# Kernel tuning notes

Hardware: AMD Instinct MI355X
Metric: run time of the kernel (lower is better)

## Reference

```python
import jax, jax.numpy as jnp
import numpy as np

N = 20000      # nodes
E = 320000     # directed edges (self-loops added inside reference)
DIN = 128      # input_dim
HID = 64       # hidden_dim
H = 4          # num_heads
B = 16         # graphs in batch
OUT = 1        # output_dim
NEG_SLOPE = 0.2


def setup_inputs() -> dict:
    key = jax.random.key(0)
    ks = jax.random.split(key, 20)
    p = lambda k, shape: (jax.random.normal(k, shape, jnp.float32) * 0.05)
    x = jax.random.normal(ks[0], (N, DIN), jnp.float32)
    edge_index = jax.random.randint(ks[1], (2, E), 0, N, dtype=jnp.int64)
    batch = jnp.sort(jax.random.randint(ks[2], (N,), 0, B, dtype=jnp.int64))
    return {
        "x": x, "edge_index": edge_index, "batch": batch,
        # gat1: DIN -> (H, HID), concat
        "W1": p(ks[3], (DIN, H * HID)), "as1": p(ks[4], (H, HID)), "ad1": p(ks[5], (H, HID)), "b1": jnp.zeros((H * HID,), jnp.float32),
        # gat2: H*HID -> (H, HID), concat
        "W2": p(ks[6], (H * HID, H * HID)), "as2": p(ks[7], (H, HID)), "ad2": p(ks[8], (H, HID)), "b2": jnp.zeros((H * HID,), jnp.float32),
        # gat_out: H*HID -> (1, HID), mean (concat=False)
        "W3": p(ks[9], (H * HID, HID)), "as3": p(ks[10], (1, HID)), "ad3": p(ks[11], (1, HID)), "b3": jnp.zeros((HID,), jnp.float32),
        "wp": p(ks[12], (HID, 1)), "bp": jnp.zeros((1,), jnp.float32),
        "wr": p(ks[13], (HID, OUT)), "br": jnp.zeros((OUT,), jnp.float32),
    }


def _gat_layer(x, W, a_src, a_dst, bias, src, dst, heads, concat):
    n = x.shape[0]
    h = (x @ W).reshape(n, heads, -1)                      # [N,H,C]
    e_src = (h * a_src).sum(-1)                            # [N,H]
    e_dst = (h * a_dst).sum(-1)                            # [N,H]
    e = jax.nn.leaky_relu(e_src[src] + e_dst[dst], NEG_SLOPE)  # [Etot,H]
    # segment softmax over destination node (self-loops guarantee non-empty)
    m = jax.ops.segment_max(e, dst, num_segments=n)
    e = jnp.exp(e - m[dst])
    den = jax.ops.segment_sum(e, dst, num_segments=n)
    alpha = e / den[dst]                                   # [Etot,H]
    out = jax.ops.segment_sum(h[src] * alpha[..., None], dst, num_segments=n)  # [N,H,C]
    out = out.reshape(n, -1) if concat else out.mean(axis=1)
    return out + bias


def reference(x, edge_index, batch, W1, as1, ad1, b1, W2, as2, ad2, b2,
              W3, as3, ad3, b3, wp, bp, wr, br):
    n = x.shape[0]
    loops = jnp.arange(n, dtype=edge_index.dtype)
    src = jnp.concatenate([edge_index[0], loops])
    dst = jnp.concatenate([edge_index[1], loops])

    h = jax.nn.elu(_gat_layer(x, W1, as1, ad1, b1, src, dst, H, True))
    h = jax.nn.elu(_gat_layer(h, W2, as2, ad2, b2, src, dst, H, True))
    h = jax.nn.elu(_gat_layer(h, W3, as3, ad3, b3, src, dst, 1, False))  # [N,HID]

    attn = jax.nn.sigmoid(h @ wp + bp)                     # [N,1]
    hw = h * attn                                          # [N,HID]
    sums = jax.ops.segment_sum(hw, batch, num_segments=B)  # [B,HID]
    counts = jax.ops.segment_sum(jnp.ones((n,), hw.dtype), batch, num_segments=B)
    pooled = sums / jnp.maximum(counts, 1.0)[:, None]
    return pooled @ wr + br                                # [B,OUT]
```

## Files before the change

### kernel.cpp

```cpp
#include <hip/hip_runtime.h>


typedef unsigned short u16;
typedef __attribute__((ext_vector_type(8))) short bf16x8;
typedef __attribute__((ext_vector_type(4))) float f32x4;

__device__ __forceinline__ u16 bf16rn(float x) {
    unsigned u = __float_as_uint(x);
    u += 0x7FFFu + ((u >> 16) & 1u);
    return (u16)(u >> 16);
}
__device__ __forceinline__ float bf16f(u16 h) {
    return __uint_as_float(((unsigned)h) << 16);
}

__device__ __forceinline__ void gload16(const u16* g, u16* l) {
    __builtin_amdgcn_global_load_lds(
        (const __attribute__((address_space(1))) unsigned int*)g,
        (__attribute__((address_space(3))) unsigned int*)l, 16, 0, 0);
}

__global__ void edge_hist_k(const int* __restrict__ ei, int E, int n, int* __restrict__ deg) {
    int i = blockIdx.x * blockDim.x + threadIdx.x;
    if (i >= E + n) return;
    int dst = (i < E) ? ei[E + i] : (i - E);
    atomicAdd(&deg[dst], 1);
}

__global__ void scan_p1_k(const int* __restrict__ deg, int* __restrict__ bsum, int n) {
    __shared__ int red[256];
    int tid = threadIdx.x;
    int i = blockIdx.x * 256 + tid;
    int v = (i < n) ? deg[i] : 0;
    red[tid] = v;
    __syncthreads();
    for (int off = 128; off; off >>= 1) {
        if (tid < off) red[tid] += red[tid + off];
        __syncthreads();
    }
    if (tid == 0) bsum[blockIdx.x] = red[0];
}

__global__ __launch_bounds__(1024) void scan_p2_k(int* __restrict__ bsum, int nb) {
    __shared__ int part[1024];
    int tid = threadIdx.x;
    int v = (tid < nb) ? bsum[tid] : 0;
    part[tid] = v;
    __syncthreads();
    for (int off = 1; off < 1024; off <<= 1) {
        int t = (tid >= off) ? part[tid - off] : 0;
        __syncthreads();
        part[tid] += t;
        __syncthreads();
    }
    if (tid < nb) bsum[tid] = part[tid] - v;
}

__global__ void scan_p3_k(const int* __restrict__ deg, const int* __restrict__ bsum,
                          int* __restrict__ rowptr, int* __restrict__ cursor, int n) {
    __shared__ int part[256];
    int tid = threadIdx.x;
    int i = blockIdx.x * 256 + tid;
    int v = (i < n) ? deg[i] : 0;
    part[tid] = v;
    __syncthreads();
    for (int off = 1; off < 256; off <<= 1) {
        int t = (tid >= off) ? part[tid - off] : 0;
        __syncthreads();
        part[tid] += t;
        __syncthreads();
    }
    int excl = part[tid] - v + bsum[blockIdx.x];
    if (i < n) { rowptr[i] = excl; cursor[i] = excl; }
    if (i == n - 1) rowptr[n] = excl + v;
}

__global__ void edge_scatter_k(const int* __restrict__ ei, int E, int n,
                               int* __restrict__ cursor, int* __restrict__ srcs) {
    int i = blockIdx.x * blockDim.x + threadIdx.x;
    if (i >= E + n) return;
    int src, dst;
    if (i < E) { src = ei[i]; dst = ei[E + i]; }
    else       { src = i - E; dst = src; }
    int pos = atomicAdd(&cursor[dst], 1);
    srcs[pos] = src;
}

__global__ void split_bf16_k(const float* __restrict__ in, u16* __restrict__ hi,
                             u16* __restrict__ lo, int n4) {
    int i = blockIdx.x * 256 + threadIdx.x;
    if (i >= n4) return;
    float4 v = reinterpret_cast<const float4*>(in)[i];
    u16 hx = bf16rn(v.x), hy = bf16rn(v.y), hz = bf16rn(v.z), hw = bf16rn(v.w);
    ushort4 H = make_ushort4(hx, hy, hz, hw);
    ushort4 L = make_ushort4(bf16rn(v.x - bf16f(hx)), bf16rn(v.y - bf16f(hy)),
                             bf16rn(v.z - bf16f(hz)), bf16rn(v.w - bf16f(hw)));
    reinterpret_cast<ushort4*>(hi)[i] = H;
    reinterpret_cast<ushort4*>(lo)[i] = L;
}

__global__ void splitT_bf16_k(const float* __restrict__ W, u16* __restrict__ thi,
                              u16* __restrict__ tlo, int K, int Nn) {
    int idx = blockIdx.x * 256 + threadIdx.x;
    if (idx >= K * Nn) return;
    int k = idx / Nn, nn = idx - k * Nn;
    float v = W[idx];
    u16 h = bf16rn(v);
    u16 l = bf16rn(v - bf16f(h));
    thi[(size_t)nn * K + k] = h;
    tlo[(size_t)nn * K + k] = l;
}

template <int NF>
__global__ __launch_bounds__(256) void gemm_lds_k(
        const u16* __restrict__ Ahi, const u16* __restrict__ Alo,
        const u16* __restrict__ Bthi, const u16* __restrict__ Btlo,
        float* __restrict__ C,
        const float* __restrict__ a_src, const float* __restrict__ a_dst,
        float* __restrict__ esrc, float* __restrict__ edst,
        int M, int Nn, int K) {
    __shared__ u16 Ah[2][4][64 * 8];
    __shared__ u16 Al[2][4][64 * 8];
    const int mb = (M + 63) >> 6;
    const int mi = blockIdx.x % mb;
    const int ni = blockIdx.x / mb;
    const int m0 = mi * 64;
    const int n0 = ni * (NF * 64);
    const int tid = threadIdx.x;
    const int wv = tid >> 6;
    const int lane = tid & 63;
    const int rr = lane & 15;
    const int kg = lane >> 4;

    int srow = m0 + lane; if (srow > M - 1) srow = M - 1;
    const u16* sh = Ahi + (size_t)srow * K + wv * 8;
    const u16* sl = Alo + (size_t)srow * K + wv * 8;

    const u16* pbh[NF];
    const u16* pbl[NF];
#pragma unroll
    for (int nf = 0; nf < NF; ++nf) {
        int col = n0 + (wv * NF + nf) * 16 + rr;
        pbh[nf] = Bthi + (size_t)col * K + kg * 8;
        pbl[nf] = Btlo + (size_t)col * K + kg * 8;
    }

    f32x4 acc[4][NF];
#pragma unroll
    for (int mf = 0; mf < 4; ++mf)
#pragma unroll
        for (int nf = 0; nf < NF; ++nf) acc[mf][nf] = (f32x4){0.f, 0.f, 0.f, 0.f};

    bf16x8 bhc[NF], blc[NF], bhn[NF], bln[NF];
#pragma unroll
    for (int nf = 0; nf < NF; ++nf) {
        bhc[nf] = *reinterpret_cast<const bf16x8*>(pbh[nf]);
        blc[nf] = *reinterpret_cast<const bf16x8*>(pbl[nf]);
    }
    gload16(sh, &Ah[0][wv][0]);
    gload16(sl, &Al[0][wv][0]);
    __syncthreads();

    const int NT = K >> 5;
    for (int t = 0; t < NT; ++t) {
        const int cur = t & 1;
        if (t + 1 < NT) {
            const int kc = (t + 1) << 5;
#pragma unroll
            for (int nf = 0; nf < NF; ++nf) {
                bhn[nf] = *reinterpret_cast<const bf16x8*>(pbh[nf] + kc);
                bln[nf] = *reinterpret_cast<const bf16x8*>(pbl[nf] + kc);
            }
            gload16(sh + kc, &Ah[cur ^ 1][wv][0]);
            gload16(sl + kc, &Al[cur ^ 1][wv][0]);
        }
        bf16x8 ah[4], al[4];
#pragma unroll
        for (int mf = 0; mf < 4; ++mf) {
            ah[mf] = *reinterpret_cast<const bf16x8*>(&Ah[cur][kg][(mf * 16 + rr) * 8]);
            al[mf] = *reinterpret_cast<const bf16x8*>(&Al[cur][kg][(mf * 16 + rr) * 8]);
        }
#pragma unroll
        for (int mf = 0; mf < 4; ++mf)
#pragma unroll
            for (int nf = 0; nf < NF; ++nf) {
                acc[mf][nf] = __builtin_amdgcn_mfma_f32_16x16x32_bf16(ah[mf], bhc[nf], acc[mf][nf], 0, 0, 0);
                acc[mf][nf] = __builtin_amdgcn_mfma_f32_16x16x32_bf16(ah[mf], blc[nf], acc[mf][nf], 0, 0, 0);
                acc[mf][nf] = __builtin_amdgcn_mfma_f32_16x16x32_bf16(al[mf], bhc[nf], acc[mf][nf], 0, 0, 0);
            }
#pragma unroll
        for (int nf = 0; nf < NF; ++nf) { bhc[nf] = bhn[nf]; blc[nf] = bln[nf]; }
        __syncthreads();
    }

#pragma unroll
    for (int mf = 0; mf < 4; ++mf)
#pragma unroll
        for (int nf = 0; nf < NF; ++nf) {
            int col = n0 + (wv * NF + nf) * 16 + rr;
            float* cb = C + ((size_t)(col >> 6) * M) * 64 + (col & 63);
#pragma unroll
            for (int rg = 0; rg < 4; ++rg) {
                int row = m0 + mf * 16 + kg * 4 + rg;
                if (row < M) cb[(size_t)row * 64] = acc[mf][nf][rg];
            }
        }

    float asv[NF], adv[NF];
#pragma unroll
    for (int nf = 0; nf < NF; ++nf) {
        int col = n0 + (wv * NF + nf) * 16 + rr;
        asv[nf] = a_src[col];
        adv[nf] = a_dst[col];
    }
    float ps[4][4], pd[4][4];
#pragma unroll
    for (int mf = 0; mf < 4; ++mf)
#pragma unroll
        for (int rg = 0; rg < 4; ++rg) {
            float s = 0.f, dvv = 0.f;
#pragma unroll
            for (int nf = 0; nf < NF; ++nf) {
                s = fmaf(acc[mf][nf][rg], asv[nf], s);
                dvv = fmaf(acc[mf][nf][rg], adv[nf], dvv);
            }
#pragma unroll
            for (int off = 1; off < 16; off <<= 1) {
                s += __shfl_xor(s, off);
                dvv += __shfl_xor(dvv, off);
            }
            ps[mf][rg] = s;
            pd[mf][rg] = dvv;
        }
    float* sm_src = (float*)&Ah[0][0][0];
    float* sm_dst = sm_src + 256;
    if (rr == 0) {
#pragma unroll
        for (int mf = 0; mf < 4; ++mf)
#pragma unroll
            for (int rg = 0; rg < 4; ++rg) {
                int rl = mf * 16 + kg * 4 + rg;
                sm_src[wv * 64 + rl] = ps[mf][rg];
                sm_dst[wv * 64 + rl] = pd[mf][rg];
            }
    }
    __syncthreads();
    if (tid < 64) {
        int row = m0 + tid;
        if (row < M) {
            const int HTOT = Nn >> 6;
            constexpr int WPH = 4 / NF;
#pragma unroll
            for (int hl = 0; hl < NF; ++hl) {
                float es = 0.f, edv = 0.f;
#pragma unroll
                for (int w = 0; w < WPH; ++w) {
                    es += sm_src[(hl * WPH + w) * 64 + tid];
                    edv += sm_dst[(hl * WPH + w) * 64 + tid];
                }
                int hg = ni * NF + hl;
                esrc[(size_t)row * HTOT + hg] = es;
                edst[(size_t)row * HTOT + hg] = edv;
            }
        }
    }
}

__global__ __launch_bounds__(256) void gat_aggregate_hm_k(
        const float* __restrict__ hm, const float* __restrict__ esrc,
        const float* __restrict__ edst, const int* __restrict__ rowptr,
        const int* __restrict__ srcs, const float* __restrict__ bias,
        u16* __restrict__ ghi, u16* __restrict__ glo, int n) {
    __shared__ int2 swb[4][64];
    int wv = threadIdx.x >> 6;
    int d = blockIdx.x * 4 + wv;
    int lane = threadIdx.x & 63;
    int hh = blockIdx.y;
    if (d >= n) return;
    const float* hbase = hm + (size_t)hh * n * 64;
    const int es = lane >> 4;
    const int cq = lane & 15;
    int2* swv = swb[wv];
    float ed = edst[d * 4 + hh];
    int lo = rowptr[d], hi = rowptr[d + 1];
    float4 acc = make_float4(0.f, 0.f, 0.f, 0.f);
    float den = 0.f;
    for (int base = lo; base < hi; base += 64) {
        int cnt = min(64, hi - base);
        int idx = base + lane;
        int s = srcs[(idx < hi) ? idx : lo];
        float e = esrc[s * 4 + hh] + ed;
        e = (e >= 0.f) ? e : 0.2f * e;
        float w = (lane < cnt) ? __expf(e) : 0.f;
        float ws = w;
#pragma unroll
        for (int off = 1; off < 64; off <<= 1) ws += __shfl_xor(ws, off);
        den += ws;
        swv[lane] = make_int2(s, __float_as_int(w));
        auto ROW = [&](int2 sv) -> float4 {
            return *reinterpret_cast<const float4*>(&hbase[(size_t)sv.x * 64 + cq * 4]);
        };
        int2 s0 = swv[es], s1 = swv[4 + es], s2 = swv[8 + es], s3 = swv[12 + es];
        float4 p0 = ROW(s0), p1 = ROW(s1), p2 = ROW(s2), p3 = ROW(s3);
        for (int j = 0; j < cnt; j += 16) {
            int2 t0 = s0, t1 = s1, t2 = s2, t3 = s3;
            float4 q0 = p0, q1 = p1, q2 = p2, q3 = p3;
            s0 = swv[(j + 16 + es) & 63];
            s1 = swv[(j + 20 + es) & 63];
            s2 = swv[(j + 24 + es) & 63];
            s3 = swv[(j + 28 + es) & 63];
            p0 = ROW(s0); p1 = ROW(s1); p2 = ROW(s2); p3 = ROW(s3);
            float w0 = __int_as_float(t0.y), w1 = __int_as_float(t1.y);
            float w2 = __int_as_float(t2.y), w3 = __int_as_float(t3.y);
            acc.x = fmaf(w0, q0.x, acc.x); acc.y = fmaf(w0, q0.y, acc.y);
            acc.z = fmaf(w0, q0.z, acc.z); acc.w = fmaf(w0, q0.w, acc.w);
            acc.x = fmaf(w1, q1.x, acc.x); acc.y = fmaf(w1, q1.y, acc.y);
            acc.z = fmaf(w1, q1.z, acc.z); acc.w = fmaf(w1, q1.w, acc.w);
            acc.x = fmaf(w2, q2.x, acc.x); acc.y = fmaf(w2, q2.y, acc.y);
            acc.z = fmaf(w2, q2.z, acc.z); acc.w = fmaf(w2, q2.w, acc.w);
            acc.x = fmaf(w3, q3.x, acc.x); acc.y = fmaf(w3, q3.y, acc.y);
            acc.z = fmaf(w3, q3.z, acc.z); acc.w = fmaf(w3, q3.w, acc.w);
        }
    }
    acc.x += __shfl_xor(acc.x, 16); acc.x += __shfl_xor(acc.x, 32);
    acc.y += __shfl_xor(acc.y, 16); acc.y += __shfl_xor(acc.y, 32);
    acc.z += __shfl_xor(acc.z, 16); acc.z += __shfl_xor(acc.z, 32);
    acc.w += __shfl_xor(acc.w, 16); acc.w += __shfl_xor(acc.w, 32);
    if (es == 0) {
        int c0 = hh * 64 + cq * 4;
        float inv = 1.f / den;
        float4 bv = *reinterpret_cast<const float4*>(&bias[c0]);
        float4 o;
        o.x = acc.x * inv + bv.x;
        o.y = acc.y * inv + bv.y;
        o.z = acc.z * inv + bv.z;
        o.w = acc.w * inv + bv.w;
        o.x = (o.x > 0.f) ? o.x : expm1f(o.x);
        o.y = (o.y > 0.f) ? o.y : expm1f(o.y);
        o.z = (o.z > 0.f) ? o.z : expm1f(o.z);
        o.w = (o.w > 0.f) ? o.w : expm1f(o.w);
        u16 hx = bf16rn(o.x), hy = bf16rn(o.y), hz = bf16rn(o.z), hw = bf16rn(o.w);
        ushort4 H = make_ushort4(hx, hy, hz, hw);
        ushort4 L = make_ushort4(bf16rn(o.x - bf16f(hx)), bf16rn(o.y - bf16f(hy)),
                                 bf16rn(o.z - bf16f(hz)), bf16rn(o.w - bf16f(hw)));
        *reinterpret_cast<ushort4*>(&ghi[(size_t)d * 256 + c0]) = H;
        *reinterpret_cast<ushort4*>(&glo[(size_t)d * 256 + c0]) = L;
    }
}

__global__ __launch_bounds__(256) void gat_aggregate1_attn_k(
        const float* __restrict__ hin, const float* __restrict__ esrc,
        const float* __restrict__ edst, const int* __restrict__ rowptr,
        const int* __restrict__ srcs, const float* __restrict__ bias,
        const float* __restrict__ wp, const float* __restrict__ bp,
        float* __restrict__ gout, float* __restrict__ attn, int n) {
    __shared__ int2 swb[4][64];
    int wv = threadIdx.x >> 6;
    int d = blockIdx.x * 4 + wv;
    int lane = threadIdx.x & 63;
    if (d >= n) return;
    const int es = lane >> 4;
    const int cq = lane & 15;
    int2* swv = swb[wv];
    float ed = edst[d];
    int lo = rowptr[d], hi = rowptr[d + 1];
    float4 acc = make_float4(0.f, 0.f, 0.f, 0.f);
    float den = 0.f;
    for (int base = lo; base < hi; base += 64) {
        int cnt = min(64, hi - base);
        int idx = base + lane;
        int s = srcs[(idx < hi) ? idx : lo];
        float e = esrc[s] + ed;
        e = (e >= 0.f) ? e : 0.2f * e;
        float w = (lane < cnt) ? __expf(e) : 0.f;
        float ws = w;
#pragma unroll
        for (int off = 1; off < 64; off <<= 1) ws += __shfl_xor(ws, off);
        den += ws;
        swv[lane] = make_int2(s, __float_as_int(w));
        auto ROW = [&](int2 sv) -> float4 {
            return *reinterpret_cast<const float4*>(&hin[(size_t)sv.x * 64 + cq * 4]);
        };
        int2 s0 = swv[es], s1 = swv[4 + es], s2 = swv[8 + es], s3 = swv[12 + es];
        float4 p0 = ROW(s0), p1 = ROW(s1), p2 = ROW(s2), p3 = ROW(s3);
        for (int j = 0; j < cnt; j += 16) {
            int2 t0 = s0, t1 = s1, t2 = s2, t3 = s3;
            float4 q0 = p0, q1 = p1, q2 = p2, q3 = p3;
            s0 = swv[(j + 16 + es) & 63];
            s1 = swv[(j + 20 + es) & 63];
            s2 = swv[(j + 24 + es) & 63];
            s3 = swv[(j + 28 + es) & 63];
            p0 = ROW(s0); p1 = ROW(s1); p2 = ROW(s2); p3 = ROW(s3);
            float w0 = __int_as_float(t0.y), w1 = __int_as_float(t1.y);
            float w2 = __int_as_float(t2.y), w3 = __int_as_float(t3.y);
            acc.x = fmaf(w0, q0.x, acc.x); acc.y = fmaf(w0, q0.y, acc.y);
            acc.z = fmaf(w0, q0.z, acc.z); acc.w = fmaf(w0, q0.w, acc.w);
            acc.x = fmaf(w1, q1.x, acc.x); acc.y = fmaf(w1, q1.y, acc.y);
            acc.z = fmaf(w1, q1.z, acc.z); acc.w = fmaf(w1, q1.w, acc.w);
            acc.x = fmaf(w2, q2.x, acc.x); acc.y = fmaf(w2, q2.y, acc.y);
            acc.z = fmaf(w2, q2.z, acc.z); acc.w = fmaf(w2, q2.w, acc.w);
            acc.x = fmaf(w3, q3.x, acc.x); acc.y = fmaf(w3, q3.y, acc.y);
            acc.z = fmaf(w3, q3.z, acc.z); acc.w = fmaf(w3, q3.w, acc.w);
        }
    }
    acc.x += __shfl_xor(acc.x, 16); acc.x += __shfl_xor(acc.x, 32);
    acc.y += __shfl_xor(acc.y, 16); acc.y += __shfl_xor(acc.y, 32);
    acc.z += __shfl_xor(acc.z, 16); acc.z += __shfl_xor(acc.z, 32);
    acc.w += __shfl_xor(acc.w, 16); acc.w += __shfl_xor(acc.w, 32);
    int c0 = cq * 4;
    float inv = 1.f / den;
    float4 bv = *reinterpret_cast<const float4*>(&bias[c0]);
    float4 o;
    o.x = acc.x * inv + bv.x;
    o.y = acc.y * inv + bv.y;
    o.z = acc.z * inv + bv.z;
    o.w = acc.w * inv + bv.w;
    o.x = (o.x > 0.f) ? o.x : expm1f(o.x);
    o.y = (o.y > 0.f) ? o.y : expm1f(o.y);
    o.z = (o.z > 0.f) ? o.z : expm1f(o.z);
    o.w = (o.w > 0.f) ? o.w : expm1f(o.w);
    if (es == 0)
        *reinterpret_cast<float4*>(&gout[(size_t)d * 64 + c0]) = o;
    float4 wv4 = *reinterpret_cast<const float4*>(&wp[c0]);
    float v = o.x * wv4.x + o.y * wv4.y + o.z * wv4.z + o.w * wv4.w;
#pragma unroll
    for (int off = 1; off < 16; off <<= 1) v += __shfl_xor(v, off);
    if (lane == 0) attn[d] = 1.f / (1.f + __expf(-(v + bp[0])));
}

__global__ void pool_partial_k(const float* __restrict__ g3, const float* __restrict__ attn,
                               const int* __restrict__ batch, int n, float* __restrict__ sums) {
    int wid = blockIdx.x * (blockDim.x >> 6) + (threadIdx.x >> 6);
    int lane = threadIdx.x & 63;
    int nwaves = gridDim.x * (blockDim.x >> 6);
    int per = (n + nwaves - 1) / nwaves;
    int i0 = wid * per;
    int i1 = i0 + per;
    if (i1 > n) i1 = n;
    if (i0 >= i1) return;
    int cur = batch[i0];
    float acc = 0.f;
    for (int i = i0; i < i1; ++i) {
        int b = batch[i];
        if (b != cur) {
            atomicAdd(&sums[cur * 64 + lane], acc);
            acc = 0.f;
            cur = b;
        }
        acc += g3[(size_t)i * 64 + lane] * attn[i];
    }
    atomicAdd(&sums[cur * 64 + lane], acc);
}

__global__ void regress_k(const float* __restrict__ sums, const int* __restrict__ batch, int n,
                          const float* __restrict__ wr, const float* __restrict__ br,
                          float* __restrict__ out, int B) {
    int b = threadIdx.x >> 6;
    int lane = threadIdx.x & 63;
    if (b >= B) return;
    int lo = 0, hi = n;
    while (lo < hi) { int mid = (lo + hi) >> 1; if (batch[mid] < b) lo = mid + 1; else hi = mid; }
    int seg_lo = lo;
    lo = 0; hi = n;
    while (lo < hi) { int mid = (lo + hi) >> 1; if (batch[mid] < b + 1) lo = mid + 1; else hi = mid; }
    float cnt = (float)(lo - seg_lo);
    if (cnt < 1.f) cnt = 1.f;
    float v = (sums[b * 64 + lane] / cnt) * wr[lane];
#pragma unroll
    for (int off = 32; off; off >>= 1) v += __shfl_xor(v, off);
    if (lane == 0) out[b] = v + br[0];
}

extern "C" void kernel_launch(void* const* d_in, const int* in_sizes, int n_in,
                              void* d_out, int out_size, void* d_ws, size_t ws_size,
                              hipStream_t stream) {
    const float* x   = (const float*)d_in[0];
    const int*   ei  = (const int*)d_in[1];
    const int*   bat = (const int*)d_in[2];
    const float* W1  = (const float*)d_in[3];
    const float* as1 = (const float*)d_in[4];
    const float* ad1 = (const float*)d_in[5];
    const float* b1  = (const float*)d_in[6];
    const float* W2  = (const float*)d_in[7];
    const float* as2 = (const float*)d_in[8];
    const float* ad2 = (const float*)d_in[9];
    const float* b2  = (const float*)d_in[10];
    const float* W3  = (const float*)d_in[11];
    const float* as3 = (const float*)d_in[12];
    const float* ad3 = (const float*)d_in[13];
    const float* b3  = (const float*)d_in[14];
    const float* wp  = (const float*)d_in[15];
    const float* bp  = (const float*)d_in[16];
    const float* wr  = (const float*)d_in[17];
    const float* br  = (const float*)d_in[18];
    float* out = (float*)d_out;

    const int N    = in_sizes[2];
    const int E    = in_sizes[1] / 2;
    const int DIN  = in_sizes[0] / N;
    const int Etot = E + N;
    const int Bc   = out_size;

    char* ws = (char*)d_ws;
    size_t off = 0;
    auto alloc = [&](size_t bytes) {
        void* p = ws + off;
        off = (off + bytes + 255) & ~(size_t)255;
        return p;
    };
    int*   deg    = (int*)alloc((size_t)N * 4);
    int*   rowptr = (int*)alloc((size_t)(N + 1) * 4);
    int*   cursor = (int*)alloc((size_t)N * 4);
    int*   bsum   = (int*)alloc((size_t)1024 * 4);
    int*   srcs   = (int*)alloc((size_t)Etot * 4);
    float* bufA   = (float*)alloc((size_t)N * 256 * 4);
    u16*   Ahi    = (u16*)alloc((size_t)N * 256 * 2);
    u16*   Alo    = (u16*)alloc((size_t)N * 256 * 2);
    float* h3     = (float*)alloc((size_t)N * 64 * 4);
    float* g3     = (float*)alloc((size_t)N * 64 * 4);
    float* esrc   = (float*)alloc((size_t)N * 4 * 4);
    float* edst   = (float*)alloc((size_t)N * 4 * 4);
    float* attn   = (float*)alloc((size_t)N * 4);
    float* sums   = (float*)alloc((size_t)Bc * 64 * 4);
    u16*   w1hi   = (u16*)alloc((size_t)256 * DIN * 2);
    u16*   w1lo   = (u16*)alloc((size_t)256 * DIN * 2);
    u16*   w2hi   = (u16*)alloc((size_t)256 * 256 * 2);
    u16*   w2lo   = (u16*)alloc((size_t)256 * 256 * 2);
    u16*   w3hi   = (u16*)alloc((size_t)64 * 256 * 2);
    u16*   w3lo   = (u16*)alloc((size_t)64 * 256 * 2);
    (void)ws_size;

    hipMemsetAsync(deg, 0, (size_t)N * 4, stream);
    int eb = (Etot + 255) / 256;
    int nb = (N + 255) / 256;
    edge_hist_k<<<eb, 256, 0, stream>>>(ei, E, N, deg);
    scan_p1_k<<<nb, 256, 0, stream>>>(deg, bsum, N);
    scan_p2_k<<<1, 1024, 0, stream>>>(bsum, nb);
    scan_p3_k<<<nb, 256, 0, stream>>>(deg, bsum, rowptr, cursor, N);
    edge_scatter_k<<<eb, 256, 0, stream>>>(ei, E, N, cursor, srcs);

    splitT_bf16_k<<<(DIN * 256 + 255) / 256, 256, 0, stream>>>(W1, w1hi, w1lo, DIN, 256);
    splitT_bf16_k<<<(256 * 256 + 255) / 256, 256, 0, stream>>>(W2, w2hi, w2lo, 256, 256);
    splitT_bf16_k<<<(256 * 64 + 255) / 256, 256, 0, stream>>>(W3, w3hi, w3lo, 256, 64);
    split_bf16_k<<<(N * DIN / 4 + 255) / 256, 256, 0, stream>>>(x, Ahi, Alo, N * DIN / 4);

    const int mb = (N + 63) / 64;
    int nb4 = (N + 3) / 4;
    dim3 agg_grid(nb4, 4);

    gemm_lds_k<2><<<mb * 2, 256, 0, stream>>>(Ahi, Alo, w1hi, w1lo, bufA, as1, ad1, esrc, edst, N, 256, DIN);
    gat_aggregate_hm_k<<<agg_grid, 256, 0, stream>>>(bufA, esrc, edst, rowptr, srcs, b1, Ahi, Alo, N);

    gemm_lds_k<2><<<mb * 2, 256, 0, stream>>>(Ahi, Alo, w2hi, w2lo, bufA, as2, ad2, esrc, edst, N, 256, 256);
    gat_aggregate_hm_k<<<agg_grid, 256, 0, stream>>>(bufA, esrc, edst, rowptr, srcs, b2, Ahi, Alo, N);

    gemm_lds_k<1><<<mb, 256, 0, stream>>>(Ahi, Alo, w3hi, w3lo, h3, as3, ad3, esrc, edst, N, 64, 256);
    gat_aggregate1_attn_k<<<nb4, 256, 0, stream>>>(h3, esrc, edst, rowptr, srcs, b3, wp, bp, g3, attn, N);

    hipMemsetAsync(sums, 0, (size_t)Bc * 64 * 4, stream);
    pool_partial_k<<<256, 256, 0, stream>>>(g3, attn, bat, N, sums);
    regress_k<<<1, 1024, 0, stream>>>(sums, bat, N, wr, br, out, Bc);
}
```

Before: 251.0 us.

## Process two destination nodes per wave with up-front gathers in GAT aggregation

The aggregation kernels now assign two destination nodes to each wavefront. For the first 64 edges of each node, up to 8 neighbour-row loads per node are issued before the attention weights are computed, so the two nodes' memory traffic overlaps with each other and with the exp and reduction work. Neighbour lists longer than 64 edges go through a helper that handles one chunk at a time. This raises memory-level parallelism and halves the grid, at the cost of higher register pressure (16 float4 prefetch registers) and predicated code.

```diff
diff --git a/kernel.cpp b/kernel.cpp
--- a/kernel.cpp
+++ b/kernel.cpp
@@ -266,166 +266,368 @@
     }
 }
 
-__global__ __launch_bounds__(256) void gat_aggregate_hm_k(
+#define ROWQ(SW, J, HB) \
+    (*reinterpret_cast<const float4*>(&HB[(size_t)SW[(J) + es].x * 64 + cq * 4]))
+
+#define FMA4(ACC, WK, R) \
+    ACC.x = fmaf(WK, R.x, ACC.x); ACC.y = fmaf(WK, R.y, ACC.y); \
+    ACC.z = fmaf(WK, R.z, ACC.z); ACC.w = fmaf(WK, R.w, ACC.w);
+
+#define STEPK(SW, CNT, K, R, ACC) \
+    if (CNT > 4 * (K)) { float wk_ = __int_as_float(SW[4 * (K) + es].y); FMA4(ACC, wk_, R) }
+
+__device__ __forceinline__ void agg_chunk(const float* __restrict__ hb,
+        const float* __restrict__ esrc, int hstride, int hh, float ed,
+        const int* __restrict__ srcs, int base, int hi, int2* swv,
+        int lane, int es, int cq, float4& acc, float& den) {
+    int cnt = min(64, hi - base);
+    int idx = base + lane;
+    int s = srcs[(idx < hi) ? idx : base];
+    swv[lane].x = s;
+    float4 z = make_float4(0.f, 0.f, 0.f, 0.f);
+    float4 r0 = z, r1 = z, r2 = z, r3 = z, r4 = z, r5 = z, r6 = z, r7 = z;
+    r0 = ROWQ(swv, 0, hb);
+    if (cnt > 4)  r1 = ROWQ(swv, 4, hb);
+    if (cnt > 8)  r2 = ROWQ(swv, 8, hb);
+    if (cnt > 12) r3 = ROWQ(swv, 12, hb);
+    if (cnt > 16) r4 = ROWQ(swv, 16, hb);
+    if (cnt > 20) r5 = ROWQ(swv, 20, hb);
+    if (cnt > 24) r6 = ROWQ(swv, 24, hb);
+    if (cnt > 28) r7 = ROWQ(swv, 28, hb);
+    float e = esrc[s * hstride + hh] + ed;
+    e = (e >= 0.f) ? e : 0.2f * e;
+    float w = (lane < cnt) ? __expf(e) : 0.f;
+    float ws = w;
+#pragma unroll
+    for (int off = 1; off < 64; off <<= 1) ws += __shfl_xor(ws, off);
+    den += ws;
+    swv[lane].y = __float_as_int(w);
+    STEPK(swv, cnt, 0, r0, acc) STEPK(swv, cnt, 1, r1, acc)
+    STEPK(swv, cnt, 2, r2, acc) STEPK(swv, cnt, 3, r3, acc)
+    STEPK(swv, cnt, 4, r4, acc) STEPK(swv, cnt, 5, r5, acc)
+    STEPK(swv, cnt, 6, r6, acc) STEPK(swv, cnt, 7, r7, acc)
+    if (cnt > 32) {
+        r0 = ROWQ(swv, 32, hb);
+        if (cnt > 36) r1 = ROWQ(swv, 36, hb);
+        if (cnt > 40) r2 = ROWQ(swv, 40, hb);
+        if (cnt > 44) r3 = ROWQ(swv, 44, hb);
+        if (cnt > 48) r4 = ROWQ(swv, 48, hb);
+        if (cnt > 52) r5 = ROWQ(swv, 52, hb);
+        if (cnt > 56) r6 = ROWQ(swv, 56, hb);
+        if (cnt > 60) r7 = ROWQ(swv, 60, hb);
+        STEPK(swv, cnt, 8, r0, acc)  STEPK(swv, cnt, 9, r1, acc)
+        STEPK(swv, cnt, 10, r2, acc) STEPK(swv, cnt, 11, r3, acc)
+        STEPK(swv, cnt, 12, r4, acc) STEPK(swv, cnt, 13, r5, acc)
+        STEPK(swv, cnt, 14, r6, acc) STEPK(swv, cnt, 15, r7, acc)
+    }
+}
+
+__global__ __launch_bounds__(256) void gat_aggregate_hm2_k(
         const float* __restrict__ hm, const float* __restrict__ esrc,
         const float* __restrict__ edst, const int* __restrict__ rowptr,
         const int* __restrict__ srcs, const float* __restrict__ bias,
         u16* __restrict__ ghi, u16* __restrict__ glo, int n) {
-    __shared__ int2 swb[4][64];
+    __shared__ int2 swb[4][128];
     int wv = threadIdx.x >> 6;
-    int d = blockIdx.x * 4 + wv;
     int lane = threadIdx.x & 63;
     int hh = blockIdx.y;
-    if (d >= n) return;
+    int d0 = blockIdx.x * 8 + wv * 2;
+    int d1 = d0 + 1;
+    if (d0 >= n) return;
+    bool v1 = d1 < n;
     const float* hbase = hm + (size_t)hh * n * 64;
     const int es = lane >> 4;
     const int cq = lane & 15;
-    int2* swv = swb[wv];
-    float ed = edst[d * 4 + hh];
-    int lo = rowptr[d], hi = rowptr[d + 1];
-    float4 acc = make_float4(0.f, 0.f, 0.f, 0.f);
-    float den = 0.f;
-    for (int base = lo; base < hi; base += 64) {
-        int cnt = min(64, hi - base);
-        int idx = base + lane;
-        int s = srcs[(idx < hi) ? idx : lo];
-        float e = esrc[s * 4 + hh] + ed;
-        e = (e >= 0.f) ? e : 0.2f * e;
-        float w = (lane < cnt) ? __expf(e) : 0.f;
-        float ws = w;
-#pragma unroll
-        for (int off = 1; off < 64; off <<= 1) ws += __shfl_xor(ws, off);
-        den += ws;
-        swv[lane] = make_int2(s, __float_as_int(w));
-        auto ROW = [&](int2 sv) -> float4 {
-            return *reinterpret_cast<const float4*>(&hbase[(size_t)sv.x * 64 + cq * 4]);
-        };
-        int2 s0 = swv[es], s1 = swv[4 + es], s2 = swv[8 + es], s3 = swv[12 + es];
-        float4 p0 = ROW(s0), p1 = ROW(s1), p2 = ROW(s2), p3 = ROW(s3);
-        for (int j = 0; j < cnt; j += 16) {
-            int2 t0 = s0, t1 = s1, t2 = s2, t3 = s3;
-            float4 q0 = p0, q1 = p1, q2 = p2, q3 = p3;
-            s0 = swv[(j + 16 + es) & 63];
-            s1 = swv[(j + 20 + es) & 63];
-            s2 = swv[(j + 24 + es) & 63];
-            s3 = swv[(j + 28 + es) & 63];
-            p0 = ROW(s0); p1 = ROW(s1); p2 = ROW(s2); p3 = ROW(s3);
-            float w0 = __int_as_float(t0.y), w1 = __int_as_float(t1.y);
-            float w2 = __int_as_float(t2.y), w3 = __int_as_float(t3.y);
-            acc.x = fmaf(w0, q0.x, acc.x); acc.y = fmaf(w0, q0.y, acc.y);
-            acc.z = fmaf(w0, q0.z, acc.z); acc.w = fmaf(w0, q0.w, acc.w);
-            acc.x = fmaf(w1, q1.x, acc.x); acc.y = fmaf(w1, q1.y, acc.y);
-            acc.z = fmaf(w1, q1.z, acc.z); acc.w = fmaf(w1, q1.w, acc.w);
-            acc.x = fmaf(w2, q2.x, acc.x); acc.y = fmaf(w2, q2.y, acc.y);
-            acc.z = fmaf(w2, q2.z, acc.z); acc.w = fmaf(w2, q2.w, acc.w);
-            acc.x = fmaf(w3, q3.x, acc.x); acc.y = fmaf(w3, q3.y, acc.y);
-            acc.z = fmaf(w3, q3.z, acc.z); acc.w = fmaf(w3, q3.w, acc.w);
-        }
-    }
-    acc.x += __shfl_xor(acc.x, 16); acc.x += __shfl_xor(acc.x, 32);
-    acc.y += __shfl_xor(acc.y, 16); acc.y += __shfl_xor(acc.y, 32);
-    acc.z += __shfl_xor(acc.z, 16); acc.z += __shfl_xor(acc.z, 32);
-    acc.w += __shfl_xor(acc.w, 16); acc.w += __shfl_xor(acc.w, 32);
+    int2* sw0 = swb[wv];
+    int2* sw1 = swb[wv] + 64;
+    int lo0 = rowptr[d0], hi0 = rowptr[d0 + 1];
+    int hi1 = v1 ? rowptr[d0 + 2] : hi0;
+    int lo1 = hi0;
+    int cnt0 = min(64, hi0 - lo0);
+    int cnt1 = v1 ? min(64, hi1 - lo1) : 0;
+    float ed0 = edst[d0 * 4 + hh];
+    float ed1 = v1 ? edst[d1 * 4 + hh] : 0.f;
+    int i0 = lo0 + lane;
+    int s0 = srcs[(i0 < hi0) ? i0 : lo0];
+    int i1 = lo1 + lane;
+    int s1 = (cnt1 > 0) ? srcs[(i1 < hi1) ? i1 : lo1] : 0;
+    sw0[lane].x = s0;
+    sw1[lane].x = s1;
+    float4 z = make_float4(0.f, 0.f, 0.f, 0.f);
+    float4 a0 = z, a1 = z, a2 = z, a3 = z, a4 = z, a5 = z, a6 = z, a7 = z;
+    float4 b0 = z, b1 = z, b2 = z, b3 = z, b4 = z, b5 = z, b6 = z, b7 = z;
+    a0 = ROWQ(sw0, 0, hbase);
+    if (cnt0 > 4)  a1 = ROWQ(sw0, 4, hbase);
+    if (cnt0 > 8)  a2 = ROWQ(sw0, 8, hbase);
+    if (cnt0 > 12) a3 = ROWQ(sw0, 12, hbase);
+    if (cnt0 > 16) a4 = ROWQ(sw0, 16, hbase);
+    if (cnt0 > 20) a5 = ROWQ(sw0, 20, hbase);
+    if (cnt0 > 24) a6 = ROWQ(sw0, 24, hbase);
+    if (cnt0 > 28) a7 = ROWQ(sw0, 28, hbase);
+    if (cnt1 > 0)  b0 = ROWQ(sw1, 0, hbase);
+    if (cnt1 > 4)  b1 = ROWQ(sw1, 4, hbase);
+    if (cnt1 > 8)  b2 = ROWQ(sw1, 8, hbase);
+    if (cnt1 > 12) b3 = ROWQ(sw1, 12, hbase);
+    if (cnt1 > 16) b4 = ROWQ(sw1, 16, hbase);
+    if (cnt1 > 20) b5 = ROWQ(sw1, 20, hbase);
+    if (cnt1 > 24) b6 = ROWQ(sw1, 24, hbase);
+    if (cnt1 > 28) b7 = ROWQ(sw1, 28, hbase);
+    float e0 = esrc[s0 * 4 + hh] + ed0;
+    e0 = (e0 >= 0.f) ? e0 : 0.2f * e0;
+    float w0 = (lane < cnt0) ? __expf(e0) : 0.f;
+    float e1 = esrc[s1 * 4 + hh] + ed1;
+    e1 = (e1 >= 0.f) ? e1 : 0.2f * e1;
+    float w1 = (lane < cnt1) ? __expf(e1) : 0.f;
+    float den0 = w0, den1 = w1;
+#pragma unroll
+    for (int off = 1; off < 64; off <<= 1) {
+        den0 += __shfl_xor(den0, off);
+        den1 += __shfl_xor(den1, off);
+    }
+    sw0[lane].y = __float_as_int(w0);
+    sw1[lane].y = __float_as_int(w1);
+    float4 acc0 = z, acc1 = z;
+    STEPK(sw0, cnt0, 0, a0, acc0) STEPK(sw0, cnt0, 1, a1, acc0)
+    STEPK(sw0, cnt0, 2, a2, acc0) STEPK(sw0, cnt0, 3, a3, acc0)
+    STEPK(sw0, cnt0, 4, a4, acc0) STEPK(sw0, cnt0, 5, a5, acc0)
+    STEPK(sw0, cnt0, 6, a6, acc0) STEPK(sw0, cnt0, 7, a7, acc0)
+    STEPK(sw1, cnt1, 0, b0, acc1) STEPK(sw1, cnt1, 1, b1, acc1)
+    STEPK(sw1, cnt1, 2, b2, acc1) STEPK(sw1, cnt1, 3, b3, acc1)
+    STEPK(sw1, cnt1, 4, b4, acc1) STEPK(sw1, cnt1, 5, b5, acc1)
+    STEPK(sw1, cnt1, 6, b6, acc1) STEPK(sw1, cnt1, 7, b7, acc1)
+    if (cnt0 > 32) {
+        a0 = ROWQ(sw0, 32, hbase);
+        if (cnt0 > 36) a1 = ROWQ(sw0, 36, hbase);
+        if (cnt0 > 40) a2 = ROWQ(sw0, 40, hbase);
+        if (cnt0 > 44) a3 = ROWQ(sw0, 44, hbase);
+        if (cnt0 > 48) a4 = ROWQ(sw0, 48, hbase);
+        if (cnt0 > 52) a5 = ROWQ(sw0, 52, hbase);
+        if (cnt0 > 56) a6 = ROWQ(sw0, 56, hbase);
+        if (cnt0 > 60) a7 = ROWQ(sw0, 60, hbase);
+        STEPK(sw0, cnt0, 8, a0, acc0)  STEPK(sw0, cnt0, 9, a1, acc0)
+        STEPK(sw0, cnt0, 10, a2, acc0) STEPK(sw0, cnt0, 11, a3, acc0)
+        STEPK(sw0, cnt0, 12, a4, acc0) STEPK(sw0, cnt0, 13, a5, acc0)
+        STEPK(sw0, cnt0, 14, a6, acc0) STEPK(sw0, cnt0, 15, a7, acc0)
+    }
+    if (cnt1 > 32) {
+        b0 = ROWQ(sw1, 32, hbase);
+        if (cnt1 > 36) b1 = ROWQ(sw1, 36, hbase);
+        if (cnt1 > 40) b2 = ROWQ(sw1, 40, hbase);
+        if (cnt1 > 44) b3 = ROWQ(sw1, 44, hbase);
+        if (cnt1 > 48) b4 = ROWQ(sw1, 48, hbase);
+        if (cnt1 > 52) b5 = ROWQ(sw1, 52, hbase);
+        if (cnt1 > 56) b6 = ROWQ(sw1, 56, hbase);
+        if (cnt1 > 60) b7 = ROWQ(sw1, 60, hbase);
+        STEPK(sw1, cnt1, 8, b0, acc1)  STEPK(sw1, cnt1, 9, b1, acc1)
+        STEPK(sw1, cnt1, 10, b2, acc1) STEPK(sw1, cnt1, 11, b3, acc1)
+        STEPK(sw1, cnt1, 12, b4, acc1) STEPK(sw1, cnt1, 13, b5, acc1)
+        STEPK(sw1, cnt1, 14, b6, acc1) STEPK(sw1, cnt1, 15, b7, acc1)
+    }
+    for (int base = lo0 + 64; base < hi0; base += 64)
+        agg_chunk(hbase, esrc, 4, hh, ed0, srcs, base, hi0, sw0, lane, es, cq, acc0, den0);
+    for (int base = lo1 + 64; base < hi1; base += 64)
+        agg_chunk(hbase, esrc, 4, hh, ed1, srcs, base, hi1, sw1, lane, es, cq, acc1, den1);
+    acc0.x += __shfl_xor(acc0.x, 16); acc0.x += __shfl_xor(acc0.x, 32);
+    acc0.y += __shfl_xor(acc0.y, 16); acc0.y += __shfl_xor(acc0.y, 32);
+    acc0.z += __shfl_xor(acc0.z, 16); acc0.z += __shfl_xor(acc0.z, 32);
+    acc0.w += __shfl_xor(acc0.w, 16); acc0.w += __shfl_xor(acc0.w, 32);
+    acc1.x += __shfl_xor(acc1.x, 16); acc1.x += __shfl_xor(acc1.x, 32);
+    acc1.y += __shfl_xor(acc1.y, 16); acc1.y += __shfl_xor(acc1.y, 32);
+    acc1.z += __shfl_xor(acc1.z, 16); acc1.z += __shfl_xor(acc1.z, 32);
+    acc1.w += __shfl_xor(acc1.w, 16); acc1.w += __shfl_xor(acc1.w, 32);
     if (es == 0) {
         int c0 = hh * 64 + cq * 4;
-        float inv = 1.f / den;
         float4 bv = *reinterpret_cast<const float4*>(&bias[c0]);
-        float4 o;
-        o.x = acc.x * inv + bv.x;
-        o.y = acc.y * inv + bv.y;
-        o.z = acc.z * inv + bv.z;
-        o.w = acc.w * inv + bv.w;
-        o.x = (o.x > 0.f) ? o.x : expm1f(o.x);
-        o.y = (o.y > 0.f) ? o.y : expm1f(o.y);
-        o.z = (o.z > 0.f) ? o.z : expm1f(o.z);
-        o.w = (o.w > 0.f) ? o.w : expm1f(o.w);
-        u16 hx = bf16rn(o.x), hy = bf16rn(o.y), hz = bf16rn(o.z), hw = bf16rn(o.w);
-        ushort4 H = make_ushort4(hx, hy, hz, hw);
-        ushort4 L = make_ushort4(bf16rn(o.x - bf16f(hx)), bf16rn(o.y - bf16f(hy)),
-                                 bf16rn(o.z - bf16f(hz)), bf16rn(o.w - bf16f(hw)));
-        *reinterpret_cast<ushort4*>(&ghi[(size_t)d * 256 + c0]) = H;
-        *reinterpret_cast<ushort4*>(&glo[(size_t)d * 256 + c0]) = L;
-    }
-}
-
-__global__ __launch_bounds__(256) void gat_aggregate1_attn_k(
+        {
+            float inv = 1.f / den0;
+            float4 o;
+            o.x = acc0.x * inv + bv.x;
+            o.y = acc0.y * inv + bv.y;
+            o.z = acc0.z * inv + bv.z;
+            o.w = acc0.w * inv + bv.w;
+            o.x = (o.x > 0.f) ? o.x : expm1f(o.x);
+            o.y = (o.y > 0.f) ? o.y : expm1f(o.y);
+            o.z = (o.z > 0.f) ? o.z : expm1f(o.z);
+            o.w = (o.w > 0.f) ? o.w : expm1f(o.w);
+            u16 hx = bf16rn(o.x), hy = bf16rn(o.y), hz = bf16rn(o.z), hw = bf16rn(o.w);
+            ushort4 H = make_ushort4(hx, hy, hz, hw);
+            ushort4 L = make_ushort4(bf16rn(o.x - bf16f(hx)), bf16rn(o.y - bf16f(hy)),
+                                     bf16rn(o.z - bf16f(hz)), bf16rn(o.w - bf16f(hw)));
+            *reinterpret_cast<ushort4*>(&ghi[(size_t)d0 * 256 + c0]) = H;
+            *reinterpret_cast<ushort4*>(&glo[(size_t)d0 * 256 + c0]) = L;
+        }
+        if (v1) {
+            float inv = 1.f / den1;
+            float4 o;
+            o.x = acc1.x * inv + bv.x;
+            o.y = acc1.y * inv + bv.y;
+            o.z = acc1.z * inv + bv.z;
+            o.w = acc1.w * inv + bv.w;
+            o.x = (o.x > 0.f) ? o.x : expm1f(o.x);
+            o.y = (o.y > 0.f) ? o.y : expm1f(o.y);
+            o.z = (o.z > 0.f) ? o.z : expm1f(o.z);
+            o.w = (o.w > 0.f) ? o.w : expm1f(o.w);
+            u16 hx = bf16rn(o.x), hy = bf16rn(o.y), hz = bf16rn(o.z), hw = bf16rn(o.w);
+            ushort4 H = make_ushort4(hx, hy, hz, hw);
+            ushort4 L = make_ushort4(bf16rn(o.x - bf16f(hx)), bf16rn(o.y - bf16f(hy)),
+                                     bf16rn(o.z - bf16f(hz)), bf16rn(o.w - bf16f(hw)));
+            *reinterpret_cast<ushort4*>(&ghi[(size_t)d1 * 256 + c0]) = H;
+            *reinterpret_cast<ushort4*>(&glo[(size_t)d1 * 256 + c0]) = L;
+        }
+    }
+}
+
+__global__ __launch_bounds__(256) void gat_aggregate1_attn2_k(
         const float* __restrict__ hin, const float* __restrict__ esrc,
         const float* __restrict__ edst, const int* __restrict__ rowptr,
         const int* __restrict__ srcs, const float* __restrict__ bias,
         const float* __restrict__ wp, const float* __restrict__ bp,
         float* __restrict__ gout, float* __restrict__ attn, int n) {
-    __shared__ int2 swb[4][64];
+    __shared__ int2 swb[4][128];
     int wv = threadIdx.x >> 6;
-    int d = blockIdx.x * 4 + wv;
     int lane = threadIdx.x & 63;
-    if (d >= n) return;
+    int d0 = blockIdx.x * 8 + wv * 2;
+    int d1 = d0 + 1;
+    if (d0 >= n) return;
+    bool v1 = d1 < n;
     const int es = lane >> 4;
     const int cq = lane & 15;
-    int2* swv = swb[wv];
-    float ed = edst[d];
-    int lo = rowptr[d], hi = rowptr[d + 1];
-    float4 acc = make_float4(0.f, 0.f, 0.f, 0.f);
-    float den = 0.f;
-    for (int base = lo; base < hi; base += 64) {
-        int cnt = min(64, hi - base);
-        int idx = base + lane;
-        int s = srcs[(idx < hi) ? idx : lo];
-        float e = esrc[s] + ed;
-        e = (e >= 0.f) ? e : 0.2f * e;
-        float w = (lane < cnt) ? __expf(e) : 0.f;
-        float ws = w;
-#pragma unroll
-        for (int off = 1; off < 64; off <<= 1) ws += __shfl_xor(ws, off);
-        den += ws;
-        swv[lane] = make_int2(s, __float_as_int(w));
-        auto ROW = [&](int2 sv) -> float4 {
-            return *reinterpret_cast<const float4*>(&hin[(size_t)sv.x * 64 + cq * 4]);
-        };
-        int2 s0 = swv[es], s1 = swv[4 + es], s2 = swv[8 + es], s3 = swv[12 + es];
-        float4 p0 = ROW(s0), p1 = ROW(s1), p2 = ROW(s2), p3 = ROW(s3);
-        for (int j = 0; j < cnt; j += 16) {
-            int2 t0 = s0, t1 = s1, t2 = s2, t3 = s3;
-            float4 q0 = p0, q1 = p1, q2 = p2, q3 = p3;
-            s0 = swv[(j + 16 + es) & 63];
-            s1 = swv[(j + 20 + es) & 63];
-            s2 = swv[(j + 24 + es) & 63];
-            s3 = swv[(j + 28 + es) & 63];
-            p0 = ROW(s0); p1 = ROW(s1); p2 = ROW(s2); p3 = ROW(s3);
-            float w0 = __int_as_float(t0.y), w1 = __int_as_float(t1.y);
-            float w2 = __int_as_float(t2.y), w3 = __int_as_float(t3.y);
-            acc.x = fmaf(w0, q0.x, acc.x); acc.y = fmaf(w0, q0.y, acc.y);
-            acc.z = fmaf(w0, q0.z, acc.z); acc.w = fmaf(w0, q0.w, acc.w);
-            acc.x = fmaf(w1, q1.x, acc.x); acc.y = fmaf(w1, q1.y, acc.y);
-            acc.z = fmaf(w1, q1.z, acc.z); acc.w = fmaf(w1, q1.w, acc.w);
-            acc.x = fmaf(w2, q2.x, acc.x); acc.y = fmaf(w2, q2.y, acc.y);
-            acc.z = fmaf(w2, q2.z, acc.z); acc.w = fmaf(w2, q2.w, acc.w);
-            acc.x = fmaf(w3, q3.x, acc.x); acc.y = fmaf(w3, q3.y, acc.y);
-            acc.z = fmaf(w3, q3.z, acc.z); acc.w = fmaf(w3, q3.w, acc.w);
-        }
-    }
-    acc.x += __shfl_xor(acc.x, 16); acc.x += __shfl_xor(acc.x, 32);
-    acc.y += __shfl_xor(acc.y, 16); acc.y += __shfl_xor(acc.y, 32);
-    acc.z += __shfl_xor(acc.z, 16); acc.z += __shfl_xor(acc.z, 32);
-    acc.w += __shfl_xor(acc.w, 16); acc.w += __shfl_xor(acc.w, 32);
+    int2* sw0 = swb[wv];
+    int2* sw1 = swb[wv] + 64;
+    int lo0 = rowptr[d0], hi0 = rowptr[d0 + 1];
+    int hi1 = v1 ? rowptr[d0 + 2] : hi0;
+    int lo1 = hi0;
+    int cnt0 = min(64, hi0 - lo0);
+    int cnt1 = v1 ? min(64, hi1 - lo1) : 0;
+    float ed0 = edst[d0];
+    float ed1 = v1 ? edst[d1] : 0.f;
+    int i0 = lo0 + lane;
+    int s0 = srcs[(i0 < hi0) ? i0 : lo0];
+    int i1 = lo1 + lane;
+    int s1 = (cnt1 > 0) ? srcs[(i1 < hi1) ? i1 : lo1] : 0;
+    sw0[lane].x = s0;
+    sw1[lane].x = s1;
+    float4 z = make_float4(0.f, 0.f, 0.f, 0.f);
+    float4 a0 = z, a1 = z, a2 = z, a3 = z, a4 = z, a5 = z, a6 = z, a7 = z;
+    float4 b0 = z, b1 = z, b2 = z, b3 = z, b4 = z, b5 = z, b6 = z, b7 = z;
+    a0 = ROWQ(sw0, 0, hin);
+    if (cnt0 > 4)  a1 = ROWQ(sw0, 4, hin);
+    if (cnt0 > 8)  a2 = ROWQ(sw0, 8, hin);
+    if (cnt0 > 12) a3 = ROWQ(sw0, 12, hin);
+    if (cnt0 > 16) a4 = ROWQ(sw0, 16, hin);
+    if (cnt0 > 20) a5 = ROWQ(sw0, 20, hin);
+    if (cnt0 > 24) a6 = ROWQ(sw0, 24, hin);
+    if (cnt0 > 28) a7 = ROWQ(sw0, 28, hin);
+    if (cnt1 > 0)  b0 = ROWQ(sw1, 0, hin);
+    if (cnt1 > 4)  b1 = ROWQ(sw1, 4, hin);
+    if (cnt1 > 8)  b2 = ROWQ(sw1, 8, hin);
+    if (cnt1 > 12) b3 = ROWQ(sw1, 12, hin);
+    if (cnt1 > 16) b4 = ROWQ(sw1, 16, hin);
+    if (cnt1 > 20) b5 = ROWQ(sw1, 20, hin);
+    if (cnt1 > 24) b6 = ROWQ(sw1, 24, hin);
+    if (cnt1 > 28) b7 = ROWQ(sw1, 28, hin);
+    float e0 = esrc[s0] + ed0;
+    e0 = (e0 >= 0.f) ? e0 : 0.2f * e0;
+    float w0 = (lane < cnt0) ? __expf(e0) : 0.f;
+    float e1 = esrc[s1] + ed1;
+    e1 = (e1 >= 0.f) ? e1 : 0.2f * e1;
+    float w1 = (lane < cnt1) ? __expf(e1) : 0.f;
+    float den0 = w0, den1 = w1;
+#pragma unroll
+    for (int off = 1; off < 64; off <<= 1) {
+        den0 += __shfl_xor(den0, off);
+        den1 += __shfl_xor(den1, off);
+    }
+    sw0[lane].y = __float_as_int(w0);
+    sw1[lane].y = __float_as_int(w1);
+    float4 acc0 = z, acc1 = z;
+    STEPK(sw0, cnt0, 0, a0, acc0) STEPK(sw0, cnt0, 1, a1, acc0)
+    STEPK(sw0, cnt0, 2, a2, acc0) STEPK(sw0, cnt0, 3, a3, acc0)
+    STEPK(sw0, cnt0, 4, a4, acc0) STEPK(sw0, cnt0, 5, a5, acc0)
+    STEPK(sw0, cnt0, 6, a6, acc0) STEPK(sw0, cnt0, 7, a7, acc0)
+    STEPK(sw1, cnt1, 0, b0, acc1) STEPK(sw1, cnt1, 1, b1, acc1)
+    STEPK(sw1, cnt1, 2, b2, acc1) STEPK(sw1, cnt1, 3, b3, acc1)
+    STEPK(sw1, cnt1, 4, b4, acc1) STEPK(sw1, cnt1, 5, b5, acc1)
+    STEPK(sw1, cnt1, 6, b6, acc1) STEPK(sw1, cnt1, 7, b7, acc1)
+    if (cnt0 > 32) {
+        a0 = ROWQ(sw0, 32, hin);
+        if (cnt0 > 36) a1 = ROWQ(sw0, 36, hin);
+        if (cnt0 > 40) a2 = ROWQ(sw0, 40, hin);
+        if (cnt0 > 44) a3 = ROWQ(sw0, 44, hin);
+        if (cnt0 > 48) a4 = ROWQ(sw0, 48, hin);
+        if (cnt0 > 52) a5 = ROWQ(sw0, 52, hin);
+        if (cnt0 > 56) a6 = ROWQ(sw0, 56, hin);
+        if (cnt0 > 60) a7 = ROWQ(sw0, 60, hin);
+        STEPK(sw0, cnt0, 8, a0, acc0)  STEPK(sw0, cnt0, 9, a1, acc0)
+        STEPK(sw0, cnt0, 10, a2, acc0) STEPK(sw0, cnt0, 11, a3, acc0)
+        STEPK(sw0, cnt0, 12, a4, acc0) STEPK(sw0, cnt0, 13, a5, acc0)
+        STEPK(sw0, cnt0, 14, a6, acc0) STEPK(sw0, cnt0, 15, a7, acc0)
+    }
+    if (cnt1 > 32) {
+        b0 = ROWQ(sw1, 32, hin);
+        if (cnt1 > 36) b1 = ROWQ(sw1, 36, hin);
+        if (cnt1 > 40) b2 = ROWQ(sw1, 40, hin);
+        if (cnt1 > 44) b3 = ROWQ(sw1, 44, hin);
+        if (cnt1 > 48) b4 = ROWQ(sw1, 48, hin);
+        if (cnt1 > 52) b5 = ROWQ(sw1, 52, hin);
+        if (cnt1 > 56) b6 = ROWQ(sw1, 56, hin);
+        if (cnt1 > 60) b7 = ROWQ(sw1, 60, hin);
+        STEPK(sw1, cnt1, 8, b0, acc1)  STEPK(sw1, cnt1, 9, b1, acc1)
+        STEPK(sw1, cnt1, 10, b2, acc1) STEPK(sw1, cnt1, 11, b3, acc1)
+        STEPK(sw1, cnt1, 12, b4, acc1) STEPK(sw1, cnt1, 13, b5, acc1)
+        STEPK(sw1, cnt1, 14, b6, acc1) STEPK(sw1, cnt1, 15, b7, acc1)
+    }
+    for (int base = lo0 + 64; base < hi0; base += 64)
+        agg_chunk(hin, esrc, 1, 0, ed0, srcs, base, hi0, sw0, lane, es, cq, acc0, den0);
+    for (int base = lo1 + 64; base < hi1; base += 64)
+        agg_chunk(hin, esrc, 1, 0, ed1, srcs, base, hi1, sw1, lane, es, cq, acc1, den1);
+    acc0.x += __shfl_xor(acc0.x, 16); acc0.x += __shfl_xor(acc0.x, 32);
+    acc0.y += __shfl_xor(acc0.y, 16); acc0.y += __shfl_xor(acc0.y, 32);
+    acc0.z += __shfl_xor(acc0.z, 16); acc0.z += __shfl_xor(acc0.z, 32);
+    acc0.w += __shfl_xor(acc0.w, 16); acc0.w += __shfl_xor(acc0.w, 32);
+    acc1.x += __shfl_xor(acc1.x, 16); acc1.x += __shfl_xor(acc1.x, 32);
+    acc1.y += __shfl_xor(acc1.y, 16); acc1.y += __shfl_xor(acc1.y, 32);
+    acc1.z += __shfl_xor(acc1.z, 16); acc1.z += __shfl_xor(acc1.z, 32);
+    acc1.w += __shfl_xor(acc1.w, 16); acc1.w += __shfl_xor(acc1.w, 32);
     int c0 = cq * 4;
-    float inv = 1.f / den;
     float4 bv = *reinterpret_cast<const float4*>(&bias[c0]);
-    float4 o;
-    o.x = acc.x * inv + bv.x;
-    o.y = acc.y * inv + bv.y;
-    o.z = acc.z * inv + bv.z;
-    o.w = acc.w * inv + bv.w;
-    o.x = (o.x > 0.f) ? o.x : expm1f(o.x);
-    o.y = (o.y > 0.f) ? o.y : expm1f(o.y);
-    o.z = (o.z > 0.f) ? o.z : expm1f(o.z);
-    o.w = (o.w > 0.f) ? o.w : expm1f(o.w);
-    if (es == 0)
-        *reinterpret_cast<float4*>(&gout[(size_t)d * 64 + c0]) = o;
     float4 wv4 = *reinterpret_cast<const float4*>(&wp[c0]);
-    float v = o.x * wv4.x + o.y * wv4.y + o.z * wv4.z + o.w * wv4.w;
-#pragma unroll
-    for (int off = 1; off < 16; off <<= 1) v += __shfl_xor(v, off);
-    if (lane == 0) attn[d] = 1.f / (1.f + __expf(-(v + bp[0])));
+    {
+        float inv = 1.f / den0;
+        float4 o;
+        o.x = acc0.x * inv + bv.x;
+        o.y = acc0.y * inv + bv.y;
+        o.z = acc0.z * inv + bv.z;
+        o.w = acc0.w * inv + bv.w;
+        o.x = (o.x > 0.f) ? o.x : expm1f(o.x);
+        o.y = (o.y > 0.f) ? o.y : expm1f(o.y);
+        o.z = (o.z > 0.f) ? o.z : expm1f(o.z);
+        o.w = (o.w > 0.f) ? o.w : expm1f(o.w);
+        if (es == 0)
+            *reinterpret_cast<float4*>(&gout[(size_t)d0 * 64 + c0]) = o;
+        float v = o.x * wv4.x + o.y * wv4.y + o.z * wv4.z + o.w * wv4.w;
+#pragma unroll
+        for (int off = 1; off < 16; off <<= 1) v += __shfl_xor(v, off);
+        if (lane == 0) attn[d0] = 1.f / (1.f + __expf(-(v + bp[0])));
+    }
+    if (v1) {
+        float inv = 1.f / den1;
+        float4 o;
+        o.x = acc1.x * inv + bv.x;
+        o.y = acc1.y * inv + bv.y;
+        o.z = acc1.z * inv + bv.z;
+        o.w = acc1.w * inv + bv.w;
+        o.x = (o.x > 0.f) ? o.x : expm1f(o.x);
+        o.y = (o.y > 0.f) ? o.y : expm1f(o.y);
+        o.z = (o.z > 0.f) ? o.z : expm1f(o.z);
+        o.w = (o.w > 0.f) ? o.w : expm1f(o.w);
+        if (es == 0)
+            *reinterpret_cast<float4*>(&gout[(size_t)d1 * 64 + c0]) = o;
+        float v = o.x * wv4.x + o.y * wv4.y + o.z * wv4.z + o.w * wv4.w;
+#pragma unroll
+        for (int off = 1; off < 16; off <<= 1) v += __shfl_xor(v, off);
+        if (lane == 0) attn[d1] = 1.f / (1.f + __expf(-(v + bp[0])));
+    }
 }
 
 __global__ void pool_partial_k(const float* __restrict__ g3, const float* __restrict__ attn,
@@ -545,17 +747,17 @@
     split_bf16_k<<<(N * DIN / 4 + 255) / 256, 256, 0, stream>>>(x, Ahi, Alo, N * DIN / 4);
 
     const int mb = (N + 63) / 64;
-    int nb4 = (N + 3) / 4;
-    dim3 agg_grid(nb4, 4);
+    int nb8 = (N + 7) / 8;
+    dim3 agg_grid(nb8, 4);
 
     gemm_lds_k<2><<<mb * 2, 256, 0, stream>>>(Ahi, Alo, w1hi, w1lo, bufA, as1, ad1, esrc, edst, N, 256, DIN);
-    gat_aggregate_hm_k<<<agg_grid, 256, 0, stream>>>(bufA, esrc, edst, rowptr, srcs, b1, Ahi, Alo, N);
+    gat_aggregate_hm2_k<<<agg_grid, 256, 0, stream>>>(bufA, esrc, edst, rowptr, srcs, b1, Ahi, Alo, N);
 
     gemm_lds_k<2><<<mb * 2, 256, 0, stream>>>(Ahi, Alo, w2hi, w2lo, bufA, as2, ad2, esrc, edst, N, 256, 256);
-    gat_aggregate_hm_k<<<agg_grid, 256, 0, stream>>>(bufA, esrc, edst, rowptr, srcs, b2, Ahi, Alo, N);
+    gat_aggregate_hm2_k<<<agg_grid, 256, 0, stream>>>(bufA, esrc, edst, rowptr, srcs, b2, Ahi, Alo, N);
 
     gemm_lds_k<1><<<mb, 256, 0, stream>>>(Ahi, Alo, w3hi, w3lo, h3, as3, ad3, esrc, edst, N, 64, 256);
-    gat_aggregate1_attn_k<<<nb4, 256, 0, stream>>>(h3, esrc, edst, rowptr, srcs, b3, wp, bp, g3, attn, N);
+    gat_aggregate1_attn2_k<<<nb8, 256, 0, stream>>>(h3, esrc, edst, rowptr, srcs, b3, wp, bp, g3, attn, N);
 
     hipMemsetAsync(sums, 0, (size_t)Bc * 64 * 4, stream);
     pool_partial_k<<<256, 256, 0, stream>>>(g3, attn, bat, N, sums);
```

After: 269.5 us. 7.4% more time.
